# Kernel optimization log

Measured on AMD Instinct MI355X. Metric: run time of the kernel, lower is better.

## Reference

```python
import jax, jax.numpy as jnp
import numpy as np

N_NODES = 50000


def setup_inputs() -> dict:
    key = jax.random.key(0)
    ks = jax.random.split(key, 5)
    d_in, d_out = 96, 96
    x = jax.random.normal(ks[0], (N_NODES, d_in), dtype=jnp.float32)
    edge_index = jax.random.randint(ks[1], (2, 800000), 0, N_NODES, dtype=jnp.int64)
    W_gcn = jax.random.normal(ks[2], (d_in, d_out), dtype=jnp.float32) / np.sqrt(d_in)
    b_gcn = jnp.zeros((d_out,), dtype=jnp.float32)
    W_lin = jax.random.normal(ks[3], (d_in, d_out), dtype=jnp.float32) / np.sqrt(d_in)
    b_lin = jnp.zeros((d_out,), dtype=jnp.float32)
    return {"x": x, "edge_index": edge_index, "W_gcn": W_gcn, "b_gcn": b_gcn,
            "W_lin": W_lin, "b_lin": b_lin}


def mish(y):
    return y * jnp.tanh(jax.nn.softplus(y))


def gcn_conv(x, edge_index, W, b):
    n = x.shape[0]
    # add self-loops (PyG GCNConv default)
    loop = jnp.arange(n, dtype=edge_index.dtype)
    src = jnp.concatenate([edge_index[0], loop])  # [E+N]
    dst = jnp.concatenate([edge_index[1], loop])
    h = x @ W  # [N, d_out]
    # symmetric normalization: deg over destination nodes of A+I
    deg = jax.ops.segment_sum(jnp.ones_like(dst, dtype=h.dtype), dst, num_segments=n)
    dinv = jnp.where(deg > 0, jax.lax.rsqrt(deg), 0.0)
    norm = dinv[src] * dinv[dst]  # [E+N]
    msg = h[src] * norm[:, None]  # gather + scale
    agg = jax.ops.segment_sum(msg, dst, num_segments=n)  # scatter-add
    return agg + b


def reference(x, edge_index, W_gcn, b_gcn, W_lin, b_lin):
    x_gcn = gcn_conv(x, edge_index, W_gcn, b_gcn)
    x_skip = x @ W_lin + b_lin
    return mish(x_gcn + x_skip)
```

## Files before the change

### kernel.cpp

```cpp
#include <hip/hip_runtime.h>
#include <hip/hip_bf16.h>
#include <math.h>

#define D 96
#define CAP 48

typedef __attribute__((ext_vector_type(8))) short bf16x8;
typedef __attribute__((ext_vector_type(4))) float f32x4;
typedef __attribute__((ext_vector_type(8))) unsigned short u16x8;

__global__ void fill_bucket_kernel(const int* __restrict__ src, const int* __restrict__ dst,
                                   int* __restrict__ cursor, unsigned short* __restrict__ bucket,
                                   int e) {
    int i = blockIdx.x * blockDim.x + threadIdx.x;
    if (i < e) {
        int d = dst[i];
        int pos = atomicAdd(&cursor[d], 1);
        if (pos < CAP) bucket[d * CAP + pos] = (unsigned short)src[i];
    }
}

__global__ void prep_w_kernel(const float* __restrict__ Wg, const float* __restrict__ Wl,
                              __hip_bfloat16* __restrict__ wT) {
    int i = blockIdx.x * 256 + threadIdx.x;
    if (i >= 192 * D) return;
    int c = i / D, k = i % D;
    float v = (c < D) ? Wg[k * D + c] : Wl[k * D + (c - D)];
    wT[i] = __float2bfloat16(v);
}

__global__ __launch_bounds__(256) void gemm_mfma_kernel(
    const float* __restrict__ x, const __hip_bfloat16* __restrict__ wT,
    const float* __restrict__ bl, const int* __restrict__ cursor,
    __hip_bfloat16* __restrict__ hp, float* __restrict__ out, int n)
{
    __shared__ __hip_bfloat16 sx[64 * D];
    __shared__ __hip_bfloat16 sw[192 * D];
    int tid = threadIdx.x;
    int rbase = blockIdx.x * 64;

    {
        const ushort4* s4 = (const ushort4*)wT;
        ushort4* d4 = (ushort4*)sw;
        for (int i = tid; i < 192 * D / 4; i += 256) d4[i] = s4[i];
    }
    for (int i = tid; i < 64 * D / 4; i += 256) {
        int r = i / (D / 4);
        int c4 = (i % (D / 4)) * 4;
        int grow = rbase + r;
        float4 v = make_float4(0.f, 0.f, 0.f, 0.f);
        if (grow < n) v = *(const float4*)&x[(size_t)grow * D + c4];
        __hip_bfloat16* dp = &sx[r * D + c4];
        dp[0] = __float2bfloat16(v.x); dp[1] = __float2bfloat16(v.y);
        dp[2] = __float2bfloat16(v.z); dp[3] = __float2bfloat16(v.w);
    }
    __syncthreads();

    int w = tid >> 6, l = tid & 63;
    int lrow = l & 15, lk = (l >> 4) * 8;

    bf16x8 a[3];
#pragma unroll
    for (int kc = 0; kc < 3; kc++)
        a[kc] = *(const bf16x8*)&sx[(w * 16 + lrow) * D + kc * 32 + lk];

    f32x4 acc[12];
#pragma unroll
    for (int ct = 0; ct < 12; ct++) acc[ct] = (f32x4){0.f, 0.f, 0.f, 0.f};

#pragma unroll
    for (int ct = 0; ct < 12; ct++) {
#pragma unroll
        for (int kc = 0; kc < 3; kc++) {
            bf16x8 b = *(const bf16x8*)&sw[(ct * 16 + lrow) * D + kc * 32 + lk];
            acc[ct] = __builtin_amdgcn_mfma_f32_16x16x32_bf16(a[kc], b, acc[ct], 0, 0, 0);
        }
    }

    int col0 = l & 15;
#pragma unroll
    for (int j = 0; j < 4; j++) {
        int row = rbase + w * 16 + (l >> 4) * 4 + j;
        if (row < n) {
            float dinv = rsqrtf((float)(cursor[row] + 1));
            size_t hb = (size_t)row * D;
#pragma unroll
            for (int ct = 0; ct < 6; ct++)
                hp[hb + ct * 16 + col0] = __float2bfloat16(acc[ct][j] * dinv);
#pragma unroll
            for (int ct = 0; ct < 6; ct++) {
                int c = ct * 16 + col0;
                out[hb + c] = acc[6 + ct][j] + bl[c];
            }
        }
    }
}

__device__ __forceinline__ float mish_f(float v) {
    float u = __expf(v);
    float t = u * u + 2.f * u;
    float m = v * t / (t + 2.f);
    return (v > 30.f) ? v : m;
}

__global__ __launch_bounds__(256) void gather_kernel(
    const __hip_bfloat16* __restrict__ hp, const int* __restrict__ cursor,
    const unsigned short* __restrict__ bucket, const float* __restrict__ bg,
    float* __restrict__ out, int n)
{
    int tid = threadIdx.x;
    int g = tid >> 5;
    int lane = tid & 31;
    int sub = lane >> 4;
    int j = lane & 15;
    bool active = (j < 12);
    int d = blockIdx.x * 8 + g;
    if (d >= n) return;

    int deg = cursor[d];
    int cnt = deg < CAP ? deg : CAP;
    const unsigned short* bk = bucket + (size_t)d * CAP;
    const unsigned short* hpu = (const unsigned short*)hp;

    float acc[8], acc2[8];
#pragma unroll
    for (int k = 0; k < 8; k++) { acc[k] = 0.f; acc2[k] = 0.f; }

    if (sub == 0 && active) {
        u16x8 v = *(const u16x8*)&hpu[(size_t)d * D + j * 8];
#pragma unroll
        for (int k = 0; k < 8; k++)
            acc[k] += __uint_as_float(((unsigned int)v[k]) << 16);
    }

    int e = sub;
    for (; e + 2 < cnt; e += 4) {
        int s0 = bk[e], s1 = bk[e + 2];
        if (active) {
            u16x8 v0 = *(const u16x8*)&hpu[(size_t)s0 * D + j * 8];
            u16x8 v1 = *(const u16x8*)&hpu[(size_t)s1 * D + j * 8];
#pragma unroll
            for (int k = 0; k < 8; k++) {
                acc[k]  += __uint_as_float(((unsigned int)v0[k]) << 16);
                acc2[k] += __uint_as_float(((unsigned int)v1[k]) << 16);
            }
        }
    }
    if (e < cnt) {
        int s0 = bk[e];
        if (active) {
            u16x8 v0 = *(const u16x8*)&hpu[(size_t)s0 * D + j * 8];
#pragma unroll
            for (int k = 0; k < 8; k++)
                acc[k] += __uint_as_float(((unsigned int)v0[k]) << 16);
        }
    }

#pragma unroll
    for (int k = 0; k < 8; k++) acc[k] += acc2[k];
#pragma unroll
    for (int k = 0; k < 8; k++) acc[k] += __shfl_xor(acc[k], 16, 32);

    if (sub == 0 && active) {
        float dinv = rsqrtf((float)(deg + 1));
        size_t ob = (size_t)d * D + j * 8;
        float4 s0 = *(const float4*)&out[ob];
        float4 s1 = *(const float4*)&out[ob + 4];
        float4 b0 = *(const float4*)&bg[j * 8];
        float4 b1 = *(const float4*)&bg[j * 8 + 4];
        float r[8];
        r[0] = mish_f(acc[0] * dinv + b0.x + s0.x);
        r[1] = mish_f(acc[1] * dinv + b0.y + s0.y);
        r[2] = mish_f(acc[2] * dinv + b0.z + s0.z);
        r[3] = mish_f(acc[3] * dinv + b0.w + s0.w);
        r[4] = mish_f(acc[4] * dinv + b1.x + s1.x);
        r[5] = mish_f(acc[5] * dinv + b1.y + s1.y);
        r[6] = mish_f(acc[6] * dinv + b1.z + s1.z);
        r[7] = mish_f(acc[7] * dinv + b1.w + s1.w);
        *(float4*)&out[ob]     = make_float4(r[0], r[1], r[2], r[3]);
        *(float4*)&out[ob + 4] = make_float4(r[4], r[5], r[6], r[7]);
    }
}

extern "C" void kernel_launch(void* const* d_in, const int* in_sizes, int n_in,
                              void* d_out, int out_size, void* d_ws, size_t ws_size,
                              hipStream_t stream)
{
    const float* x  = (const float*)d_in[0];
    const int* edge = (const int*)d_in[1];
    const float* Wg = (const float*)d_in[2];
    const float* bg = (const float*)d_in[3];
    const float* Wl = (const float*)d_in[4];
    const float* bl = (const float*)d_in[5];
    float* out = (float*)d_out;

    const int n = in_sizes[0] / D;
    const int e = in_sizes[1] / 2;
    const int* src = edge;
    const int* dst = edge + e;

    int* cursor = (int*)d_ws;
    size_t off_b = ((size_t)n * sizeof(int) + 255) & ~(size_t)255;
    __hip_bfloat16* wT = (__hip_bfloat16*)((char*)d_ws + off_b);
    off_b += (size_t)192 * D * sizeof(__hip_bfloat16);
    off_b = (off_b + 255) & ~(size_t)255;
    __hip_bfloat16* hp = (__hip_bfloat16*)((char*)d_ws + off_b);
    off_b += (size_t)n * D * sizeof(__hip_bfloat16);
    off_b = (off_b + 255) & ~(size_t)255;
    unsigned short* bucket = (unsigned short*)((char*)d_ws + off_b);

    hipMemsetAsync(cursor, 0, (size_t)n * sizeof(int), stream);
    prep_w_kernel<<<(192 * D + 255) / 256, 256, 0, stream>>>(Wg, Wl, wT);
    fill_bucket_kernel<<<(e + 255) / 256, 256, 0, stream>>>(src, dst, cursor, bucket, e);
    gemm_mfma_kernel<<<(n + 63) / 64, 256, 0, stream>>>(x, wT, bl, cursor, hp, out, n);
    gather_kernel<<<(n + 7) / 8, 256, 0, stream>>>(hp, cursor, bucket, bg, out, n);
}
```

Baseline: 174.7 us.

## Partition bucket fill by XCD, fuse memset into prep, deepen gather unroll

Fill_bucket now runs a persistent grid in which each group of blocks, mapped to one XCD by blockIdx modulo 8, scans every edge but only handles destinations in its own node range. The intent is to keep the atomics and bucket writes for a node inside one XCD's L2 and avoid cross-XCD coherence traffic, at the cost of each edge's dst being read eight times. The cursor memset is folded into the weight-prep kernel, which removes one launch. The gather loop now keeps four independent accumulators and issues four loads per step to raise memory-level parallelism, which adds register pressure.

Measured after the change: 179.6 us. +2.8%, slower.

```diff
diff --git a/kernel.cpp b/kernel.cpp
--- a/kernel.cpp
+++ b/kernel.cpp
@@ -4,29 +4,43 @@
 
 #define D 96
 #define CAP 48
+#define NXCD 8
+#define FILL_GPB 80
 
 typedef __attribute__((ext_vector_type(8))) short bf16x8;
 typedef __attribute__((ext_vector_type(4))) float f32x4;
 typedef __attribute__((ext_vector_type(8))) unsigned short u16x8;
 
-__global__ void fill_bucket_kernel(const int* __restrict__ src, const int* __restrict__ dst,
-                                   int* __restrict__ cursor, unsigned short* __restrict__ bucket,
-                                   int e) {
-    int i = blockIdx.x * blockDim.x + threadIdx.x;
-    if (i < e) {
+__global__ __launch_bounds__(256) void prep_kernel(const float* __restrict__ Wg,
+                                                   const float* __restrict__ Wl,
+                                                   __hip_bfloat16* __restrict__ wT,
+                                                   int* __restrict__ cursor, int n) {
+    int i = blockIdx.x * 256 + threadIdx.x;
+    if (i < n) cursor[i] = 0;
+    if (i < 192 * D) {
+        int c = i / D, k = i % D;
+        float v = (c < D) ? Wg[k * D + c] : Wl[k * D + (c - D)];
+        wT[i] = __float2bfloat16(v);
+    }
+}
+
+__global__ __launch_bounds__(256) void fill_bucket_kernel(
+    const int* __restrict__ src, const int* __restrict__ dst,
+    int* __restrict__ cursor, unsigned short* __restrict__ bucket,
+    int e, int n)
+{
+    int g = blockIdx.x & (NXCD - 1);
+    int bc = blockIdx.x >> 3;
+    int lo = (g * n) / NXCD;
+    int hi = ((g + 1) * n) / NXCD;
+    int stride = FILL_GPB * 256;
+    for (int i = bc * 256 + threadIdx.x; i < e; i += stride) {
         int d = dst[i];
-        int pos = atomicAdd(&cursor[d], 1);
-        if (pos < CAP) bucket[d * CAP + pos] = (unsigned short)src[i];
-    }
-}
-
-__global__ void prep_w_kernel(const float* __restrict__ Wg, const float* __restrict__ Wl,
-                              __hip_bfloat16* __restrict__ wT) {
-    int i = blockIdx.x * 256 + threadIdx.x;
-    if (i >= 192 * D) return;
-    int c = i / D, k = i % D;
-    float v = (c < D) ? Wg[k * D + c] : Wl[k * D + (c - D)];
-    wT[i] = __float2bfloat16(v);
+        if (d >= lo && d < hi) {
+            int pos = atomicAdd(&cursor[d], 1);
+            if (pos < CAP) bucket[(size_t)d * CAP + pos] = (unsigned short)src[i];
+        }
+    }
 }
 
 __global__ __launch_bounds__(256) void gemm_mfma_kernel(
@@ -122,44 +136,48 @@
     const unsigned short* bk = bucket + (size_t)d * CAP;
     const unsigned short* hpu = (const unsigned short*)hp;
 
-    float acc[8], acc2[8];
-#pragma unroll
-    for (int k = 0; k < 8; k++) { acc[k] = 0.f; acc2[k] = 0.f; }
+    float a0[8], a1[8], a2[8], a3[8];
+#pragma unroll
+    for (int k = 0; k < 8; k++) { a0[k] = 0.f; a1[k] = 0.f; a2[k] = 0.f; a3[k] = 0.f; }
 
     if (sub == 0 && active) {
         u16x8 v = *(const u16x8*)&hpu[(size_t)d * D + j * 8];
 #pragma unroll
         for (int k = 0; k < 8; k++)
-            acc[k] += __uint_as_float(((unsigned int)v[k]) << 16);
+            a0[k] += __uint_as_float(((unsigned int)v[k]) << 16);
     }
 
     int e = sub;
-    for (; e + 2 < cnt; e += 4) {
-        int s0 = bk[e], s1 = bk[e + 2];
+    for (; e + 6 < cnt; e += 8) {
+        int s0 = bk[e], s1 = bk[e + 2], s2 = bk[e + 4], s3 = bk[e + 6];
         if (active) {
             u16x8 v0 = *(const u16x8*)&hpu[(size_t)s0 * D + j * 8];
             u16x8 v1 = *(const u16x8*)&hpu[(size_t)s1 * D + j * 8];
+            u16x8 v2 = *(const u16x8*)&hpu[(size_t)s2 * D + j * 8];
+            u16x8 v3 = *(const u16x8*)&hpu[(size_t)s3 * D + j * 8];
 #pragma unroll
             for (int k = 0; k < 8; k++) {
-                acc[k]  += __uint_as_float(((unsigned int)v0[k]) << 16);
-                acc2[k] += __uint_as_float(((unsigned int)v1[k]) << 16);
+                a0[k] += __uint_as_float(((unsigned int)v0[k]) << 16);
+                a1[k] += __uint_as_float(((unsigned int)v1[k]) << 16);
+                a2[k] += __uint_as_float(((unsigned int)v2[k]) << 16);
+                a3[k] += __uint_as_float(((unsigned int)v3[k]) << 16);
             }
         }
     }
-    if (e < cnt) {
+    for (; e < cnt; e += 2) {
         int s0 = bk[e];
         if (active) {
             u16x8 v0 = *(const u16x8*)&hpu[(size_t)s0 * D + j * 8];
 #pragma unroll
             for (int k = 0; k < 8; k++)
-                acc[k] += __uint_as_float(((unsigned int)v0[k]) << 16);
-        }
-    }
-
-#pragma unroll
-    for (int k = 0; k < 8; k++) acc[k] += acc2[k];
-#pragma unroll
-    for (int k = 0; k < 8; k++) acc[k] += __shfl_xor(acc[k], 16, 32);
+                a0[k] += __uint_as_float(((unsigned int)v0[k]) << 16);
+        }
+    }
+
+#pragma unroll
+    for (int k = 0; k < 8; k++) a0[k] += (a1[k] + a2[k]) + a3[k];
+#pragma unroll
+    for (int k = 0; k < 8; k++) a0[k] += __shfl_xor(a0[k], 16, 32);
 
     if (sub == 0 && active) {
         float dinv = rsqrtf((float)(deg + 1));
@@ -169,14 +187,14 @@
         float4 b0 = *(const float4*)&bg[j * 8];
         float4 b1 = *(const float4*)&bg[j * 8 + 4];
         float r[8];
-        r[0] = mish_f(acc[0] * dinv + b0.x + s0.x);
-        r[1] = mish_f(acc[1] * dinv + b0.y + s0.y);
-        r[2] = mish_f(acc[2] * dinv + b0.z + s0.z);
-        r[3] = mish_f(acc[3] * dinv + b0.w + s0.w);
-        r[4] = mish_f(acc[4] * dinv + b1.x + s1.x);
-        r[5] = mish_f(acc[5] * dinv + b1.y + s1.y);
-        r[6] = mish_f(acc[6] * dinv + b1.z + s1.z);
-        r[7] = mish_f(acc[7] * dinv + b1.w + s1.w);
+        r[0] = mish_f(a0[0] * dinv + b0.x + s0.x);
+        r[1] = mish_f(a0[1] * dinv + b0.y + s0.y);
+        r[2] = mish_f(a0[2] * dinv + b0.z + s0.z);
+        r[3] = mish_f(a0[3] * dinv + b0.w + s0.w);
+        r[4] = mish_f(a0[4] * dinv + b1.x + s1.x);
+        r[5] = mish_f(a0[5] * dinv + b1.y + s1.y);
+        r[6] = mish_f(a0[6] * dinv + b1.z + s1.z);
+        r[7] = mish_f(a0[7] * dinv + b1.w + s1.w);
         *(float4*)&out[ob]     = make_float4(r[0], r[1], r[2], r[3]);
         *(float4*)&out[ob + 4] = make_float4(r[4], r[5], r[6], r[7]);
     }
@@ -209,9 +227,9 @@
     off_b = (off_b + 255) & ~(size_t)255;
     unsigned short* bucket = (unsigned short*)((char*)d_ws + off_b);
 
-    hipMemsetAsync(cursor, 0, (size_t)n * sizeof(int), stream);
-    prep_w_kernel<<<(192 * D + 255) / 256, 256, 0, stream>>>(Wg, Wl, wT);
-    fill_bucket_kernel<<<(e + 255) / 256, 256, 0, stream>>>(src, dst, cursor, bucket, e);
+    int prep_blocks = (n + 255) / 256;
+    prep_kernel<<<prep_blocks, 256, 0, stream>>>(Wg, Wl, wT, cursor, n);
+    fill_bucket_kernel<<<NXCD * FILL_GPB, 256, 0, stream>>>(src, dst, cursor, bucket, e, n);
     gemm_mfma_kernel<<<(n + 63) / 64, 256, 0, stream>>>(x, wT, bl, cursor, hp, out, n);
     gather_kernel<<<(n + 7) / 8, 256, 0, stream>>>(hp, cursor, bucket, bg, out, n);
 }
```
